# Optimization experiments

Measured on AMD Instinct MI355X. Metric: run time of the kernel, lower is better.

The kernel has to match this reference:

```python
import jax, jax.numpy as jnp
import numpy as np


def setup_inputs() -> dict:
    key = jax.random.key(0)
    k1, k2 = jax.random.split(key)
    B, S, I, H = 1, 1024, 512, 64
    J = I
    a = jax.random.normal(k1, (B, S, I, H), dtype=jnp.float32)
    b = jax.random.normal(k2, (B, S, J, H), dtype=jnp.float32)
    return {"a": a, "b": b}


def reference(a, b):
    # a: [*, s, i, h], b: [*, s, j, h] -> mean_s(a_sih outer b_sjh): [*, i, j, h]
    # Equivalent to the torch code's '...ish,...jsh->...ijsh' followed by mean over s,
    # but contracted directly without materializing the [*, i, j, s, h] intermediate.
    s = a.shape[-3]
    return jnp.einsum('...sih,...sjh->...ijh', a, b) / s
```

## Files before the change

kernel.cpp:

```cpp
#include <hip/hip_runtime.h>
#include <stdint.h>

typedef float f32x4 __attribute__((ext_vector_type(4)));
typedef short bf16x8 __attribute__((ext_vector_type(8)));
typedef float fragc __attribute__((ext_vector_type(4)));
typedef uint32_t u32x4 __attribute__((ext_vector_type(4)));

__device__ __forceinline__ uint32_t pk2(float lo, float hi) {
  return __builtin_amdgcn_perm(__float_as_uint(hi), __float_as_uint(lo), 0x07060302u);
}

__device__ __forceinline__ void gload16(const void* g, void* l) {
  __builtin_amdgcn_global_load_lds((const __attribute__((address_space(1))) uint32_t*)g,
                                   (__attribute__((address_space(3))) uint32_t*)l, 16, 0, 0);
}

#define WS_B_OFF 67108864ull

__global__ __launch_bounds__(512) void pack_kernel(const float* __restrict__ Ag,
                                                   const float* __restrict__ Bg,
                                                   uint8_t* __restrict__ ws) {
  const int bid  = blockIdx.x;
  const int rw   = bid & 7;
  const int kq   = (bid >> 3) & 127;
  const int side = bid >> 10;
  const int t    = threadIdx.x;

  const f32x4* S4 = (const f32x4*)(side ? Bg : Ag);
  uint8_t* dst = ws + (side ? WS_B_OFF : 0ull);

  const int base = rw * 1024 + t;
  f32x4 r1[8], r2[8];
#pragma unroll
  for (int e = 0; e < 8; ++e)
    r1[e] = __builtin_nontemporal_load(&S4[(size_t)(kq * 8 + e) * 8192 + base]);
#pragma unroll
  for (int e = 0; e < 8; ++e)
    r2[e] = __builtin_nontemporal_load(&S4[(size_t)(kq * 8 + e) * 8192 + base + 512]);

  const int hq = t & 15;
  const int ra = t >> 4;
#pragma unroll
  for (int e = 0; e < 4; ++e) {
    const int h = hq * 4 + e;
    u32x4 o1;
    o1[0] = pk2(r1[0][e], r1[1][e]); o1[1] = pk2(r1[2][e], r1[3][e]);
    o1[2] = pk2(r1[4][e], r1[5][e]); o1[3] = pk2(r1[6][e], r1[7][e]);
    uint8_t* plane = dst + ((size_t)((kq * 8 + rw) * 64 + h)) * 1024;
    *(u32x4*)(plane + ra * 16) = o1;
  }
#pragma unroll
  for (int e = 0; e < 4; ++e) {
    const int h = hq * 4 + e;
    u32x4 o2;
    o2[0] = pk2(r2[0][e], r2[1][e]); o2[1] = pk2(r2[2][e], r2[3][e]);
    o2[2] = pk2(r2[4][e], r2[5][e]); o2[3] = pk2(r2[6][e], r2[7][e]);
    uint8_t* plane = dst + ((size_t)((kq * 8 + rw) * 64 + h)) * 1024;
    *(u32x4*)(plane + (ra + 32) * 16) = o2;
  }
}

__global__ __launch_bounds__(512, 2) void gemm_kernel(const uint8_t* __restrict__ ws,
                                                      float* __restrict__ Og) {
  __shared__ alignas(16) uint8_t lds[131072];

  const int bid = blockIdx.x;
  const int x   = bid & 7;
  const int r   = bid >> 3;
  const int ip  = (x >> 2) * 2 + (r & 1);
  const int jt  = ((x >> 1) & 1) * 2 + ((r >> 1) & 1);
  const int hg  = (x & 1) * 8 + (r >> 2);
  const int i0  = ip * 128;
  const int j0  = jt * 128;
  const int hg4 = hg * 4;

  const int t = threadIdx.x, lane = t & 63, w = t >> 6;
  const int hl = w & 3, half = w >> 2;
  const int frl = lane & 15, frg = lane >> 4;

  const uint8_t* Apk = ws;
  const uint8_t* Bpk = ws + WS_B_OFF;

  fragc acc[4][8];
#pragma unroll
  for (int m = 0; m < 4; ++m)
#pragma unroll
    for (int n = 0; n < 8; ++n)
      acc[m][n] = (fragc)0.0f;

#define ISSUE(kt, b)                                                                \
  {                                                                                 \
    _Pragma("unroll") for (int k2 = 0; k2 < 2; ++k2) {                              \
      const int ko = half * 2 + k2;                                                 \
      _Pragma("unroll") for (int p = 0; p < 2; ++p) {                               \
        const size_t pa =                                                           \
            ((size_t)(((kt) * 4 + ko) * 8 + (i0 >> 6) + p) * 64 + hg4 + hl) * 1024; \
        const size_t pb =                                                           \
            ((size_t)(((kt) * 4 + ko) * 8 + (j0 >> 6) + p) * 64 + hg4 + hl) * 1024; \
        gload16(Apk + pa + lane * 16,                                               \
                lds + (b) * 65536 + hl * 8192 + ko * 2048 + p * 1024);              \
        gload16(Bpk + pb + lane * 16,                                               \
                lds + (b) * 65536 + 32768 + hl * 8192 + ko * 2048 + p * 1024);      \
      }                                                                             \
    }                                                                               \
  }

  ISSUE(0, 0)

  for (int kt = 0; kt < 32; ++kt) {
    const int b = kt & 1;
    if (kt < 31) {
      ISSUE(kt + 1, b ^ 1)
      asm volatile("s_waitcnt vmcnt(8)" ::: "memory");
    } else {
      asm volatile("s_waitcnt vmcnt(0)" ::: "memory");
    }
    __builtin_amdgcn_s_barrier();
    asm volatile("" ::: "memory");
    {
      const uint8_t* La = lds + b * 65536 + hl * 8192;
      const uint8_t* Lb = La + 32768;
      bf16x8 fb[8];
#pragma unroll
      for (int n = 0; n < 8; ++n)
        fb[n] = *(const bf16x8*)(Lb + frg * 2048 + (n * 16 + frl) * 16);
#pragma unroll
      for (int m = 0; m < 4; ++m) {
        bf16x8 fa = *(const bf16x8*)(La + frg * 2048 + (half * 64 + m * 16 + frl) * 16);
#pragma unroll
        for (int n = 0; n < 8; ++n)
          acc[m][n] = __builtin_amdgcn_mfma_f32_16x16x32_bf16(fa, fb[n], acc[m][n], 0, 0, 0);
      }
    }
    asm volatile("" ::: "memory");
    __builtin_amdgcn_s_barrier();
  }
#undef ISSUE

  const float scale = 1.0f / 1024.0f;
  const int i_r = t >> 4, jo = t & 15;
#pragma unroll
  for (int cb = 0; cb < 4; ++cb) {
    __syncthreads();
    if (half == (cb >> 1)) {
#pragma unroll
      for (int m2 = 0; m2 < 2; ++m2) {
        const int m = (cb & 1) * 2 + m2;
#pragma unroll
        for (int n = 0; n < 8; ++n) {
#pragma unroll
          for (int q = 0; q < 4; ++q) {
            const int il = m2 * 16 + frg * 4 + q;
            const int j  = n * 16 + frl;
            int byte = (il * 128 + j) * 16 + hl * 4;
            byte ^= ((byte >> 7) & 7) << 4;
            *(float*)(lds + byte) = acc[m][n][q] * scale;
          }
        }
      }
    }
    __syncthreads();
#pragma unroll
    for (int c = 0; c < 8; ++c) {
      int byte = (i_r * 128 + jo * 8 + c) * 16;
      byte ^= ((byte >> 7) & 7) << 4;
      const f32x4 v = *(const f32x4*)(lds + byte);
      *(f32x4*)(Og + ((size_t)(i0 + cb * 32 + i_r) * 512 + (j0 + jo * 8 + c)) * 64 + hg4) = v;
    }
  }
}

extern "C" void kernel_launch(void* const* d_in, const int* in_sizes, int n_in,
                              void* d_out, int out_size, void* d_ws, size_t ws_size,
                              hipStream_t stream) {
  const float* a = (const float*)d_in[0];
  const float* b = (const float*)d_in[1];
  float* out = (float*)d_out;
  uint8_t* ws = (uint8_t*)d_ws;
  pack_kernel<<<2048, 512, 0, stream>>>(a, b, ws);
  gemm_kernel<<<256, 512, 0, stream>>>(ws, out);
}
```

Baseline: 130.9 us.

## Retile GEMM to one head per block with 256x256 i-j tiles

```diff
diff --git a/kernel.cpp b/kernel.cpp
--- a/kernel.cpp
+++ b/kernel.cpp
@@ -62,47 +62,43 @@
 
 __global__ __launch_bounds__(512, 2) void gemm_kernel(const uint8_t* __restrict__ ws,
                                                       float* __restrict__ Og) {
-  __shared__ alignas(16) uint8_t lds[131072];
+  __shared__ alignas(16) uint8_t lds[65536];
 
   const int bid = blockIdx.x;
   const int x   = bid & 7;
   const int r   = bid >> 3;
-  const int ip  = (x >> 2) * 2 + (r & 1);
-  const int jt  = ((x >> 1) & 1) * 2 + ((r >> 1) & 1);
-  const int hg  = (x & 1) * 8 + (r >> 2);
-  const int i0  = ip * 128;
-  const int j0  = jt * 128;
-  const int hg4 = hg * 4;
+  const int h   = (x >> 1) * 16 + (r & 15);
+  const int tj  = x & 1;
+  const int ti  = r >> 4;
+  const int i0  = ti * 256;
+  const int j0  = tj * 256;
 
   const int t = threadIdx.x, lane = t & 63, w = t >> 6;
-  const int hl = w & 3, half = w >> 2;
+  const int wi = w >> 2, wj = w & 3;
   const int frl = lane & 15, frg = lane >> 4;
 
   const uint8_t* Apk = ws;
   const uint8_t* Bpk = ws + WS_B_OFF;
 
-  fragc acc[4][8];
+  fragc acc[8][4];
 #pragma unroll
-  for (int m = 0; m < 4; ++m)
+  for (int m = 0; m < 8; ++m)
 #pragma unroll
-    for (int n = 0; n < 8; ++n)
+    for (int n = 0; n < 4; ++n)
       acc[m][n] = (fragc)0.0f;
 
-#define ISSUE(kt, b)                                                                \
-  {                                                                                 \
-    _Pragma("unroll") for (int k2 = 0; k2 < 2; ++k2) {                              \
-      const int ko = half * 2 + k2;                                                 \
-      _Pragma("unroll") for (int p = 0; p < 2; ++p) {                               \
-        const size_t pa =                                                           \
-            ((size_t)(((kt) * 4 + ko) * 8 + (i0 >> 6) + p) * 64 + hg4 + hl) * 1024; \
-        const size_t pb =                                                           \
-            ((size_t)(((kt) * 4 + ko) * 8 + (j0 >> 6) + p) * 64 + hg4 + hl) * 1024; \
-        gload16(Apk + pa + lane * 16,                                               \
-                lds + (b) * 65536 + hl * 8192 + ko * 2048 + p * 1024);              \
-        gload16(Bpk + pb + lane * 16,                                               \
-                lds + (b) * 65536 + 32768 + hl * 8192 + ko * 2048 + p * 1024);      \
-      }                                                                             \
-    }                                                                               \
+  const int s_side = w >> 2;
+  const int s_ko   = w & 3;
+  const uint8_t* s_base = (s_side ? Bpk : Apk);
+  const int s_rw0 = (s_side ? (j0 >> 6) : (i0 >> 6));
+
+#define ISSUE(kt, b)                                                              \
+  {                                                                               \
+    _Pragma("unroll") for (int u = 0; u < 4; ++u) {                               \
+      const size_t pl = ((size_t)(((kt) * 4 + s_ko) * 8 + s_rw0 + u) * 64 + h);   \
+      gload16(s_base + pl * 1024 + lane * 16,                                     \
+              lds + (b) * 32768 + (w * 4 + u) * 1024 + lane * 16);                \
+    }                                                                             \
   }
 
   ISSUE(0, 0)
@@ -111,24 +107,25 @@
     const int b = kt & 1;
     if (kt < 31) {
       ISSUE(kt + 1, b ^ 1)
-      asm volatile("s_waitcnt vmcnt(8)" ::: "memory");
+      asm volatile("s_waitcnt vmcnt(4)" ::: "memory");
     } else {
       asm volatile("s_waitcnt vmcnt(0)" ::: "memory");
     }
     __builtin_amdgcn_s_barrier();
     asm volatile("" ::: "memory");
     {
-      const uint8_t* La = lds + b * 65536 + hl * 8192;
-      const uint8_t* Lb = La + 32768;
-      bf16x8 fb[8];
+      const uint8_t* La = lds + b * 32768;
+      const uint8_t* Lb = La + 16384;
+      bf16x8 fb[4];
 #pragma unroll
-      for (int n = 0; n < 8; ++n)
-        fb[n] = *(const bf16x8*)(Lb + frg * 2048 + (n * 16 + frl) * 16);
+      for (int n = 0; n < 4; ++n)
+        fb[n] = *(const bf16x8*)(Lb + (frg * 4 + wj) * 1024 + (n * 16 + frl) * 16);
 #pragma unroll
-      for (int m = 0; m < 4; ++m) {
-        bf16x8 fa = *(const bf16x8*)(La + frg * 2048 + (half * 64 + m * 16 + frl) * 16);
+      for (int m = 0; m < 8; ++m) {
+        bf16x8 fa = *(const bf16x8*)(La + (frg * 4 + wi * 2 + (m >> 2)) * 1024 +
+                                     ((m & 3) * 16 + frl) * 16);
 #pragma unroll
-        for (int n = 0; n < 8; ++n)
+        for (int n = 0; n < 4; ++n)
           acc[m][n] = __builtin_amdgcn_mfma_f32_16x16x32_bf16(fa, fb[n], acc[m][n], 0, 0, 0);
       }
     }
@@ -138,34 +135,16 @@
 #undef ISSUE
 
   const float scale = 1.0f / 1024.0f;
-  const int i_r = t >> 4, jo = t & 15;
 #pragma unroll
-  for (int cb = 0; cb < 4; ++cb) {
-    __syncthreads();
-    if (half == (cb >> 1)) {
+  for (int m = 0; m < 8; ++m) {
 #pragma unroll
-      for (int m2 = 0; m2 < 2; ++m2) {
-        const int m = (cb & 1) * 2 + m2;
+    for (int q = 0; q < 4; ++q) {
+      const int ig = i0 + wi * 128 + m * 16 + frg * 4 + q;
 #pragma unroll
-        for (int n = 0; n < 8; ++n) {
-#pragma unroll
-          for (int q = 0; q < 4; ++q) {
-            const int il = m2 * 16 + frg * 4 + q;
-            const int j  = n * 16 + frl;
-            int byte = (il * 128 + j) * 16 + hl * 4;
-            byte ^= ((byte >> 7) & 7) << 4;
-            *(float*)(lds + byte) = acc[m][n][q] * scale;
-          }
-        }
+      for (int n = 0; n < 4; ++n) {
+        const int jg = j0 + wj * 64 + n * 16 + frl;
+        Og[((size_t)ig * 512 + jg) * 64 + h] = acc[m][n][q] * scale;
       }
-    }
-    __syncthreads();
-#pragma unroll
-    for (int c = 0; c < 8; ++c) {
-      int byte = (i_r * 128 + jo * 8 + c) * 16;
-      byte ^= ((byte >> 7) & 7) << 4;
-      const f32x4 v = *(const f32x4*)(lds + byte);
-      *(f32x4*)(Og + ((size_t)(i0 + cb * 32 + i_r) * 512 + (j0 + jo * 8 + c)) * 64 + hg4) = v;
     }
   }
 }
```

Measured after the change: 171.7 us. 31.1% more time.
